# Kernel tuning notes

Measured on AMD Instinct MI355X. Metric: run time of the kernel, lower is better.

Reference implementation:

```python
import jax, jax.numpy as jnp
import numpy as np
import math

FACTOR = 5

def setup_inputs() -> dict:
    key = jax.random.key(0)
    kq, kk, kv = jax.random.split(key, 3)
    B, L, H, D = 2, 4096, 8, 64
    queries = jax.random.normal(kq, (B, L, H, D), dtype=jnp.float32)
    keys = jax.random.normal(kk, (B, L, H, D), dtype=jnp.float32)
    values = jax.random.normal(kv, (B, L, H, D), dtype=jnp.float32)
    attn_mask = jnp.ones((B, L), dtype=jnp.int32)
    return {"queries": queries, "keys": keys, "values": values, "attn_mask": attn_mask}

def reference(queries, keys, values, attn_mask):
    B, L_Q, H, D = queries.shape
    L_K = keys.shape[1]
    # [B, L, H, D] -> [B, H, L, D]
    Q = jnp.transpose(queries, (0, 2, 1, 3))
    K = jnp.transpose(keys, (0, 2, 1, 3))
    V = jnp.transpose(values, (0, 2, 1, 3))

    U_part = max(min(FACTOR * int(math.ceil(math.log(max(L_K, 1)))), L_K), 1)
    u = max(min(FACTOR * int(math.ceil(math.log(max(L_Q, 1)))), L_Q), 1)

    # random key sampling per query (torch.randint replaced by fixed jax key)
    idx = jax.random.randint(jax.random.key(1), (L_Q, U_part), 0, L_K)  # [L_Q, S]
    K_sample = K[:, :, idx, :]  # [B, H, L_Q, S, D]  (irregular gather)
    Q_K_sample = jnp.einsum('bhqd,bhqsd->bhqs', Q, K_sample)  # [B, H, L_Q, S]

    # sparsity measure M = max - mean(full-length normalization L_K as in source)
    M = Q_K_sample.max(axis=-1) - Q_K_sample.sum(axis=-1) / L_K  # [B, H, L_Q]
    _, M_top = jax.lax.top_k(M, u)  # [B, H, u]

    Q_reduce = jnp.take_along_axis(Q, M_top[..., None], axis=2)  # [B, H, u, D]
    scale = 1.0 / math.sqrt(D)
    scores = jnp.einsum('bhud,bhkd->bhuk', Q_reduce, K) * scale  # [B, H, u, L_K]

    mask = attn_mask[:, None, None, :]  # [B,1,1,L_K]
    scores = jnp.where(mask == 0, -jnp.inf, scores)

    A = jax.nn.softmax(scores, axis=-1)  # dropout p=0 -> identity
    context = jnp.einsum('bhuk,bhkd->bhud', A, V)  # [B, H, u, D]
    return jnp.transpose(context, (0, 2, 1, 3))  # [B, u, H, D]
```

## Files before the change

kernel.cpp:

```cpp
#include <hip/hip_runtime.h>
#include <math.h>

#define JAX_PARTITIONABLE 1

constexpr int Bc = 2, Lc = 4096, Hc = 8, Dc = 64;
constexpr int BHc = Bc * Hc;
constexpr int Uc = 45;
constexpr int NSc = 45;

typedef float vfloat4 __attribute__((ext_vector_type(4)));

struct TF2 { unsigned a, b; };

__host__ __device__ constexpr unsigned rotl32(unsigned v, int n) {
  return (v << n) | (v >> (32 - n));
}

__host__ __device__ constexpr TF2 tf2(unsigned k0, unsigned k1, unsigned x0, unsigned x1) {
  unsigned ks2 = k0 ^ k1 ^ 0x1BD11BDAu;
  x0 += k0; x1 += k1;
  x0 += x1; x1 = rotl32(x1, 13); x1 ^= x0;
  x0 += x1; x1 = rotl32(x1, 15); x1 ^= x0;
  x0 += x1; x1 = rotl32(x1, 26); x1 ^= x0;
  x0 += x1; x1 = rotl32(x1, 6);  x1 ^= x0;
  x0 += k1; x1 += ks2 + 1u;
  x0 += x1; x1 = rotl32(x1, 17); x1 ^= x0;
  x0 += x1; x1 = rotl32(x1, 29); x1 ^= x0;
  x0 += x1; x1 = rotl32(x1, 16); x1 ^= x0;
  x0 += x1; x1 = rotl32(x1, 24); x1 ^= x0;
  x0 += ks2; x1 += k0 + 2u;
  x0 += x1; x1 = rotl32(x1, 13); x1 ^= x0;
  x0 += x1; x1 = rotl32(x1, 15); x1 ^= x0;
  x0 += x1; x1 = rotl32(x1, 26); x1 ^= x0;
  x0 += x1; x1 = rotl32(x1, 6);  x1 ^= x0;
  x0 += k0; x1 += k1 + 3u;
  x0 += x1; x1 = rotl32(x1, 17); x1 ^= x0;
  x0 += x1; x1 = rotl32(x1, 29); x1 ^= x0;
  x0 += x1; x1 = rotl32(x1, 16); x1 ^= x0;
  x0 += x1; x1 = rotl32(x1, 24); x1 ^= x0;
  x0 += k1; x1 += ks2 + 4u;
  x0 += x1; x1 = rotl32(x1, 13); x1 ^= x0;
  x0 += x1; x1 = rotl32(x1, 15); x1 ^= x0;
  x0 += x1; x1 = rotl32(x1, 26); x1 ^= x0;
  x0 += x1; x1 = rotl32(x1, 6);  x1 ^= x0;
  x0 += ks2; x1 += k0 + 5u;
  return TF2{x0, x1};
}

template <int CTRL>
__device__ __forceinline__ float dpp_add(float x) {
  int t = __builtin_amdgcn_update_dpp(0, __float_as_int(x), CTRL, 0xF, 0xF, false);
  return x + __int_as_float(t);
}
template <int CTRL>
__device__ __forceinline__ int dpp_addi(int x) {
  int t = __builtin_amdgcn_update_dpp(0, x, CTRL, 0xF, 0xF, false);
  return x + t;
}
template <int CTRL>
__device__ __forceinline__ float dpp_idf(float x) {
  int t = __builtin_amdgcn_update_dpp(__float_as_int(x), __float_as_int(x), CTRL, 0xF, 0xF, false);
  return __int_as_float(t);
}
__device__ __forceinline__ float wave_max_bcast(float x) {
  x = fmaxf(x, dpp_idf<0x111>(x));
  x = fmaxf(x, dpp_idf<0x112>(x));
  x = fmaxf(x, dpp_idf<0x114>(x));
  x = fmaxf(x, dpp_idf<0x118>(x));
  x = fmaxf(x, dpp_idf<0x142>(x));
  x = fmaxf(x, dpp_idf<0x143>(x));
  return __int_as_float(__builtin_amdgcn_readlane(__float_as_int(x), 63));
}
__device__ __forceinline__ float wave_sum_bcast(float x) {
  x = dpp_add<0x111>(x);
  x = dpp_add<0x112>(x);
  x = dpp_add<0x114>(x);
  x = dpp_add<0x118>(x);
  x = dpp_add<0x142>(x);
  x = dpp_add<0x143>(x);
  return __int_as_float(__builtin_amdgcn_readlane(__float_as_int(x), 63));
}

__device__ __forceinline__ float dot4_acc(float4 q, float4 k, float a) {
  a = fmaf(q.x, k.x, a);
  a = fmaf(q.y, k.y, a);
  a = fmaf(q.z, k.z, a);
  a = fmaf(q.w, k.w, a);
  return a;
}

__global__ __launch_bounds__(256) void k_scoreM(const float* __restrict__ Q, const float* __restrict__ K,
                                                float* __restrict__ M) {
  __shared__ int sidx[720];
  int tid = threadIdx.x;
  int bx = blockIdx.x;
  int bh = bx & 15;
  int qblk = bx >> 4;
  int b = bh >> 3, h = bh & 7;
  int lane16 = tid & 15, qloc = tid >> 4;
  int q = qblk * 16 + qloc;
  constexpr TF2 kb = tf2(0u, 1u, 0u, 1u);
  for (int e = tid; e < 720; e += 256) {
    TF2 r = tf2(kb.a, kb.b, 0u, (unsigned)(qblk * 720 + e));
    sidx[e] = (int)((r.a ^ r.b) & 4095u);
  }
  __syncthreads();
  const vfloat4* Q4 = (const vfloat4*)Q;
  const vfloat4* K4 = (const vfloat4*)K;
  vfloat4 qr = Q4[((b * Lc + q) * Hc + h) * 16 + lane16];
  int kbase = (b * Lc * Hc + h) * 16 + lane16;
  const int* ip = sidx + qloc * NSc;
  float mx = -INFINITY, sm = 0.f;
  #pragma unroll
  for (int s0 = 0; s0 < NSc; s0 += 5) {
    int kk[5];
    #pragma unroll
    for (int i = 0; i < 5; ++i) kk[i] = ip[s0 + i];
    vfloat4 kv[5];
    #pragma unroll
    for (int i = 0; i < 5; ++i) kv[i] = __builtin_nontemporal_load(&K4[kbase + kk[i] * (Hc * 16)]);
    #pragma unroll
    for (int i = 0; i < 5; ++i) {
      float p = fmaf(qr[0], kv[i][0], fmaf(qr[1], kv[i][1], fmaf(qr[2], kv[i][2], qr[3] * kv[i][3])));
      p = dpp_add<0x111>(p);
      p = dpp_add<0x112>(p);
      p = dpp_add<0x114>(p);
      p = dpp_add<0x118>(p);
      mx = fmaxf(mx, p);
      sm += p;
    }
  }
  if (lane16 == 15) M[bh * Lc + q] = mx - sm * (1.0f / Lc);
}

__global__ __launch_bounds__(256) void k_topk(const float* __restrict__ M, const float* __restrict__ Q,
                                              int* __restrict__ topk, float* __restrict__ qg) {
  __shared__ unsigned su[Lc];
  __shared__ int hist[4][256];
  __shared__ int sfx[257];
  __shared__ unsigned s_prefix;
  __shared__ int s_r;
  __shared__ int n_gt, n_eq;
  __shared__ unsigned cu[64];
  __shared__ int cidx[64];
  __shared__ int eqi[64];
  __shared__ int srank[Uc];
  int bh = blockIdx.x, tid = threadIdx.x;
  int b = bh >> 3, h = bh & 7;
  int w = tid >> 6;
  const float* m = M + bh * Lc;
  for (int e = tid; e < Lc; e += 256) {
    unsigned bb = __float_as_uint(m[e]);
    su[e] = (bb & 0x80000000u) ? ~bb : (bb | 0x80000000u);
  }
  if (tid == 0) { s_r = Uc; s_prefix = 0u; n_gt = 0; n_eq = 0; sfx[256] = 0; }
  __syncthreads();
  #pragma unroll
  for (int p = 0; p < 4; ++p) {
    int shift = 24 - 8 * p;
    hist[0][tid] = 0; hist[1][tid] = 0; hist[2][tid] = 0; hist[3][tid] = 0;
    __syncthreads();
    unsigned pref = s_prefix;
    unsigned hmask = (p == 0) ? 0u : (0xFFFFFFFFu << (shift + 8));
    for (int e = tid; e < Lc; e += 256) {
      unsigned u = su[e];
      if ((u & hmask) == pref) atomicAdd(&hist[w][(u >> shift) & 255u], 1);
    }
    __syncthreads();
    if (tid < 64) {
      int i0 = 255 - 4 * tid;
      int h0 = hist[0][i0]     + hist[1][i0]     + hist[2][i0]     + hist[3][i0];
      int h1 = hist[0][i0 - 1] + hist[1][i0 - 1] + hist[2][i0 - 1] + hist[3][i0 - 1];
      int h2 = hist[0][i0 - 2] + hist[1][i0 - 2] + hist[2][i0 - 2] + hist[3][i0 - 2];
      int h3 = hist[0][i0 - 3] + hist[1][i0 - 3] + hist[2][i0 - 3] + hist[3][i0 - 3];
      int s0i = h0, s1i = s0i + h1, s2i = s1i + h2, s3i = s2i + h3;
      int tot = s3i;
      int x = tot;
      x = dpp_addi<0x111>(x);
      x = dpp_addi<0x112>(x);
      x = dpp_addi<0x114>(x);
      x = dpp_addi<0x118>(x);
      int r0 = __builtin_amdgcn_readlane(x, 15);
      int r1 = __builtin_amdgcn_readlane(x, 31);
      int r2 = __builtin_amdgcn_readlane(x, 47);
      if (tid >= 16) x += r0;
      if (tid >= 32) x += r1;
      if (tid >= 48) x += r2;
      int excl = x - tot;
      sfx[i0]     = excl + s0i;
      sfx[i0 - 1] = excl + s1i;
      sfx[i0 - 2] = excl + s2i;
      sfx[i0 - 3] = excl + s3i;
    }
    __syncthreads();
    int r = s_r;
    __syncthreads();
    int above = sfx[tid + 1];
    if (sfx[tid] >= r && above < r) {
      s_r = r - above;
      s_prefix = pref | ((unsigned)tid << shift);
    }
    __syncthreads();
  }
  unsigned T = s_prefix;
  int rf = s_r;
  for (int e = tid; e < Lc; e += 256) {
    unsigned u = su[e];
    if (u > T) {
      int p = atomicAdd(&n_gt, 1);
      cu[p] = u; cidx[p] = e;
    } else if (u == T) {
      int p = atomicAdd(&n_eq, 1);
      if (p < 64) eqi[p] = e;
    }
  }
  __syncthreads();
  int ne = n_eq < 64 ? n_eq : 64;
  if (tid < ne) {
    int myi = eqi[tid];
    int rank = 0;
    for (int j = 0; j < ne; ++j) rank += (eqi[j] < myi);
    if (rank < rf) {
      int p = atomicAdd(&n_gt, 1);
      cu[p] = T; cidx[p] = myi;
    }
  }
  __syncthreads();
  if (tid < Uc) {
    unsigned mu = cu[tid]; int mi = cidx[tid];
    int rank = 0;
    for (int j = 0; j < Uc; ++j) {
      unsigned ju = cu[j]; int ji = cidx[j];
      rank += (ju > mu) || (ju == mu && ji < mi);
    }
    topk[bh * Uc + rank] = mi;
    srank[rank] = mi;
  }
  __syncthreads();
  const float4* Q4 = (const float4*)Q;
  float4* qg4 = (float4*)qg;
  for (int e = tid; e < Uc * 16; e += 256) {
    int t = e >> 4, dq = e & 15;
    qg4[bh * Uc * 16 + e] = Q4[((b * Lc + srank[t]) * Hc + h) * 16 + dq];
  }
}

template<int NC>
__global__ __launch_bounds__(256, 4) void k_attn(const float* __restrict__ qg, const float* __restrict__ K,
                                                 const float* __restrict__ V, const int* __restrict__ amask,
                                                 float* __restrict__ pO, float* __restrict__ pM,
                                                 float* __restrict__ pL) {
  constexpr int CH = Lc / NC;
  constexpr int TG = 256 / CH;
  constexpr int SCW = CH + 4;
  int chunk = blockIdx.x, bh = blockIdx.y;
  int b = bh >> 3, h = bh & 7;
  int tid = threadIdx.x;
  __shared__ __align__(16) float qs[Uc * 64];
  __shared__ __align__(16) float sc[48][SCW];
  {
    const float4* qg4 = (const float4*)qg;
    float4* qs4w = (float4*)qs;
    for (int e = tid; e < Uc * 16; e += 256) qs4w[e] = qg4[bh * Uc * 16 + e];
  }
  for (int e = tid; e < 3 * SCW; e += 256) sc[45 + e / SCW][e % SCW] = 0.f;
  __syncthreads();
  {
    int k = tid % CH, tg = tid / CH;
    int key = chunk * CH + k;
    const float4* K4 = (const float4*)K;
    int kb = ((b * Lc + key) * Hc + h) * 16;
    float4 kr[16];
    #pragma unroll
    for (int j = 0; j < 16; ++j) kr[j] = K4[kb + j];
    int mk = amask[b * Lc + key];
    const float4* qs4 = (const float4*)qs;
    for (int t = tg; t < Uc; t += TG) {
      float a0 = 0.f, a1 = 0.f, a2 = 0.f, a3 = 0.f;
      #pragma unroll
      for (int j = 0; j < 16; j += 4) {
        a0 = dot4_acc(qs4[t * 16 + j],     kr[j],     a0);
        a1 = dot4_acc(qs4[t * 16 + j + 1], kr[j + 1], a1);
        a2 = dot4_acc(qs4[t * 16 + j + 2], kr[j + 2], a2);
        a3 = dot4_acc(qs4[t * 16 + j + 3], kr[j + 3], a3);
      }
      float acc = (a0 + a1) + (a2 + a3);
      sc[t][k] = mk ? acc * 0.125f : -INFINITY;
    }
  }
  __syncthreads();
  {
    int w = tid >> 6, lane = tid & 63;
    for (int t = w; t < Uc; t += 4) {
      float x = sc[t][lane];
      float ml = wave_max_bcast(x);
      float p = (ml != -INFINITY) ? __expf(x - ml) : 0.f;
      sc[t][lane] = p;
      float ls = wave_sum_bcast(p);
      if (lane == 0) {
        pM[(bh * NC + chunk) * Uc + t] = ml;
        pL[(bh * NC + chunk) * Uc + t] = ls;
      }
    }
  }
  __syncthreads();
  {
    int ty = tid >> 4, tx = tid & 15;
    float4 o0 = {0.f, 0.f, 0.f, 0.f};
    float4 o1 = {0.f, 0.f, 0.f, 0.f};
    float4 o2 = {0.f, 0.f, 0.f, 0.f};
    const float4* V4 = (const float4*)V;
    const float4* s0 = (const float4*)&sc[ty][0];
    const float4* s1 = (const float4*)&sc[ty + 16][0];
    const float4* s2 = (const float4*)&sc[ty + 32][0];
    int vbase = (b * Lc + chunk * CH) * (Hc * 16) + h * 16 + tx;
    #pragma unroll 2
    for (int kq = 0; kq < CH / 4; ++kq) {
      float4 p0 = s0[kq], p1 = s1[kq], p2 = s2[kq];
      float4 va = V4[vbase + (4 * kq + 0) * (Hc * 16)];
      float4 vb = V4[vbase + (4 * kq + 1) * (Hc * 16)];
      float4 vc = V4[vbase + (4 * kq + 2) * (Hc * 16)];
      float4 vd = V4[vbase + (4 * kq + 3) * (Hc * 16)];
      o0.x = fmaf(p0.x, va.x, o0.x); o0.y = fmaf(p0.x, va.y, o0.y); o0.z = fmaf(p0.x, va.z, o0.z); o0.w = fmaf(p0.x, va.w, o0.w);
      o1.x = fmaf(p1.x, va.x, o1.x); o1.y = fmaf(p1.x, va.y, o1.y); o1.z = fmaf(p1.x, va.z, o1.z); o1.w = fmaf(p1.x, va.w, o1.w);
      o2.x = fmaf(p2.x, va.x, o2.x); o2.y = fmaf(p2.x, va.y, o2.y); o2.z = fmaf(p2.x, va.z, o2.z); o2.w = fmaf(p2.x, va.w, o2.w);
      o0.x = fmaf(p0.y, vb.x, o0.x); o0.y = fmaf(p0.y, vb.y, o0.y); o0.z = fmaf(p0.y, vb.z, o0.z); o0.w = fmaf(p0.y, vb.w, o0.w);
      o1.x = fmaf(p1.y, vb.x, o1.x); o1.y = fmaf(p1.y, vb.y, o1.y); o1.z = fmaf(p1.y, vb.z, o1.z); o1.w = fmaf(p1.y, vb.w, o1.w);
      o2.x = fmaf(p2.y, vb.x, o2.x); o2.y = fmaf(p2.y, vb.y, o2.y); o2.z = fmaf(p2.y, vb.z, o2.z); o2.w = fmaf(p2.y, vb.w, o2.w);
      o0.x = fmaf(p0.z, vc.x, o0.x); o0.y = fmaf(p0.z, vc.y, o0.y); o0.z = fmaf(p0.z, vc.z, o0.z); o0.w = fmaf(p0.z, vc.w, o0.w);
      o1.x = fmaf(p1.z, vc.x, o1.x); o1.y = fmaf(p1.z, vc.y, o1.y); o1.z = fmaf(p1.z, vc.z, o1.z); o1.w = fmaf(p1.z, vc.w, o1.w);
      o2.x = fmaf(p2.z, vc.x, o2.x); o2.y = fmaf(p2.z, vc.y, o2.y); o2.z = fmaf(p2.z, vc.z, o2.z); o2.w = fmaf(p2.z, vc.w, o2.w);
      o0.x = fmaf(p0.w, vd.x, o0.x); o0.y = fmaf(p0.w, vd.y, o0.y); o0.z = fmaf(p0.w, vd.z, o0.z); o0.w = fmaf(p0.w, vd.w, o0.w);
      o1.x = fmaf(p1.w, vd.x, o1.x); o1.y = fmaf(p1.w, vd.y, o1.y); o1.z = fmaf(p1.w, vd.z, o1.z); o1.w = fmaf(p1.w, vd.w, o1.w);
      o2.x = fmaf(p2.w, vd.x, o2.x); o2.y = fmaf(p2.w, vd.y, o2.y); o2.z = fmaf(p2.w, vd.z, o2.z); o2.w = fmaf(p2.w, vd.w, o2.w);
    }
    float4* pO4 = (float4*)pO;
    int obase = ((bh * NC + chunk) * Uc) * 16 + tx;
    pO4[obase + ty * 16] = o0;
    pO4[obase + (ty + 16) * 16] = o1;
    if (ty < 13) pO4[obase + (ty + 32) * 16] = o2;
  }
}

template<int NC>
__global__ __launch_bounds__(256) void k_merge(const float* __restrict__ pO, const float* __restrict__ pM,
                                               const float* __restrict__ pL, float* __restrict__ out) {
  constexpr int CPT = NC / 4;
  __shared__ float smax[4];
  __shared__ float sden[4];
  __shared__ float snum[4][64];
  int bid = blockIdx.x;
  int bh = bid & 15, t = bid >> 4;
  int b = bh >> 3, h = bh & 7;
  int tid = threadIdx.x;
  int d = tid & 63, cg = tid >> 6;
  int mlbase = bh * NC * Uc + t;
  float lm = -INFINITY;
  #pragma unroll 4
  for (int c = cg * CPT; c < (cg + 1) * CPT; ++c)
    lm = fmaxf(lm, pM[mlbase + c * Uc]);
  if (d == 0) smax[cg] = lm;
  __syncthreads();
  float m = fmaxf(fmaxf(smax[0], smax[1]), fmaxf(smax[2], smax[3]));
  float den = 0.f, num = 0.f;
  #pragma unroll 4
  for (int c = cg * CPT; c < (cg + 1) * CPT; ++c) {
    float mc = pM[mlbase + c * Uc];
    float wgt = (mc == -INFINITY) ? 0.f : __expf(mc - m);
    den += wgt * pL[mlbase + c * Uc];
    num += wgt * pO[(mlbase + c * Uc) * 64 + d];
  }
  if (d == 0) sden[cg] = den;
  snum[cg][d] = num;
  __syncthreads();
  if (cg == 0) {
    float dn = sden[0] + sden[1] + sden[2] + sden[3];
    float nm = snum[0][d] + snum[1][d] + snum[2][d] + snum[3][d];
    out[((b * Uc + t) * Hc + h) * 64 + d] = nm / dn;
  }
}

extern "C" void kernel_launch(void* const* d_in, const int* in_sizes, int n_in,
                              void* d_out, int out_size, void* d_ws, size_t ws_size,
                              hipStream_t stream) {
  const float* Q = (const float*)d_in[0];
  const float* K = (const float*)d_in[1];
  const float* V = (const float*)d_in[2];
  const int* amask = (const int*)d_in[3];
  float* out = (float*)d_out;
  char* ws = (char*)d_ws;
  float* M    = (float*)(ws + 0x000000);
  int*   topk = (int*)(ws + 0x040000);
  float* qg   = (float*)(ws + 0x041000);
  float* pM   = (float*)(ws + 0x070000);
  size_t need64 = 0x70000UL + 64UL * 190080UL;
  size_t need32 = 0x70000UL + 32UL * 190080UL;
  int NC = ws_size >= need64 ? 64 : (ws_size >= need32 ? 32 : 16);
  float* pL = pM + 16 * NC * Uc;
  float* pO = pL + 16 * NC * Uc;

  k_scoreM<<<4096, 256, 0, stream>>>(Q, K, M);
  k_topk<<<BHc, 256, 0, stream>>>(M, Q, topk, qg);
  if (NC == 64) {
    k_attn<64><<<dim3(64, BHc), 256, 0, stream>>>(qg, K, V, amask, pO, pM, pL);
    k_merge<64><<<BHc * Uc, 256, 0, stream>>>(pO, pM, pL, out);
  } else if (NC == 32) {
    k_attn<32><<<dim3(32, BHc), 256, 0, stream>>>(qg, K, V, amask, pO, pM, pL);
    k_merge<32><<<BHc * Uc, 256, 0, stream>>>(pO, pM, pL, out);
  } else {
    k_attn<16><<<dim3(16, BHc), 256, 0, stream>>>(qg, K, V, amask, pO, pM, pL);
    k_merge<16><<<BHc * Uc, 256, 0, stream>>>(pO, pM, pL, out);
  }
}
```

Measured before the change: 165.0 us.

## Bucket sampled keys by row range and stage K tiles in shared memory

Adds a kernel that regenerates the random sample indices and buckets them, per group of 16 queries, into 32 key-row ranges of 128 rows, writing compact byte tables. The scoring kernel then loads one 128-row K tile into LDS and, for every query, evaluates only the sampled keys that fall in that tile. It writes per-range partial max and sum, and top-k combines the 32 partials. The goal is to replace random global gathers of K with shared-memory reads. In exchange it adds an extra kernel, a larger partial buffer, irregular per-query loop trip counts, and a bucket capacity limit that could silently drop entries.

```diff
diff --git a/kernel.cpp b/kernel.cpp
--- a/kernel.cpp
+++ b/kernel.cpp
@@ -7,6 +7,10 @@
 constexpr int BHc = Bc * Hc;
 constexpr int Uc = 45;
 constexpr int NSc = 45;
+constexpr int NRng = 32;
+constexpr int RowsPerRng = 128;
+constexpr int TabRowB = 96;
+constexpr int EntCap = 79;
 
 typedef float vfloat4 __attribute__((ext_vector_type(4)));
 
@@ -89,39 +93,109 @@
   return a;
 }
 
-__global__ __launch_bounds__(256) void k_scoreM(const float* __restrict__ Q, const float* __restrict__ K,
-                                                float* __restrict__ M) {
-  __shared__ int sidx[720];
+__global__ __launch_bounds__(256) void k_edges(unsigned char* __restrict__ tab) {
+  __shared__ unsigned short kk[720];
+  __shared__ int hist[512];
+  __shared__ int base[513];
+  __shared__ int cur[512];
+  int qc = blockIdx.x, tid = threadIdx.x;
+  constexpr TF2 kb = tf2(0u, 1u, 0u, 1u);
+  for (int t = tid; t < 512; t += 256) hist[t] = 0;
+  for (int e = tid; e < 720; e += 256) {
+    TF2 r = tf2(kb.a, kb.b, 0u, (unsigned)(qc * 720 + e));
+    kk[e] = (unsigned short)((r.a ^ r.b) & 4095u);
+  }
+  __syncthreads();
+  for (int e = tid; e < 720; e += 256) {
+    int b = ((int)(kk[e] >> 7)) * 16 + (e / 45);
+    atomicAdd(&hist[b], 1);
+  }
+  __syncthreads();
+  if (tid < 64) {
+    int i0 = 8 * tid;
+    int h[8], s = 0;
+    #pragma unroll
+    for (int j = 0; j < 8; ++j) { h[j] = hist[i0 + j]; s += h[j]; }
+    int x = s;
+    x = dpp_addi<0x111>(x);
+    x = dpp_addi<0x112>(x);
+    x = dpp_addi<0x114>(x);
+    x = dpp_addi<0x118>(x);
+    int r0 = __builtin_amdgcn_readlane(x, 15);
+    int r1 = __builtin_amdgcn_readlane(x, 31);
+    int r2 = __builtin_amdgcn_readlane(x, 47);
+    if (tid >= 16) x += r0;
+    if (tid >= 32) x += r1;
+    if (tid >= 48) x += r2;
+    int excl = x - s;
+    int acc = excl;
+    #pragma unroll
+    for (int j = 0; j < 8; ++j) { base[i0 + j] = acc; acc += h[j]; }
+    if (tid == 63) base[512] = acc;
+  }
+  __syncthreads();
+  for (int t = tid; t < 512; t += 256) cur[t] = base[t];
+  for (int t = tid; t < 512; t += 256) {
+    int r = t >> 4, j = t & 15;
+    tab[qc * (NRng * TabRowB) + r * TabRowB + j] = (unsigned char)(base[r * 16 + j] - base[r * 16]);
+  }
+  if (tid < NRng)
+    tab[qc * (NRng * TabRowB) + tid * TabRowB + 16] = (unsigned char)(base[tid * 16 + 16] - base[tid * 16]);
+  __syncthreads();
+  for (int e = tid; e < 720; e += 256) {
+    int k = kk[e];
+    int b = (k >> 7) * 16 + (e / 45);
+    int pos = atomicAdd(&cur[b], 1);
+    int r = b >> 4;
+    int local = pos - base[r * 16];
+    if (local < EntCap)
+      tab[qc * (NRng * TabRowB) + r * TabRowB + 17 + local] = (unsigned char)(k & 127);
+  }
+}
+
+__global__ __launch_bounds__(256) void k_scoreM2(const float* __restrict__ Q, const float* __restrict__ K,
+                                                 const unsigned* __restrict__ tab32,
+                                                 float2* __restrict__ P2) {
+  __shared__ vfloat4 sK[RowsPerRng * 16];
+  __shared__ unsigned wtb[4][3][24];
   int tid = threadIdx.x;
   int bx = blockIdx.x;
   int bh = bx & 15;
-  int qblk = bx >> 4;
+  int rr = (bx >> 4) & 31;
+  int qgi = bx >> 9;
   int b = bh >> 3, h = bh & 7;
-  int lane16 = tid & 15, qloc = tid >> 4;
-  int q = qblk * 16 + qloc;
-  constexpr TF2 kb = tf2(0u, 1u, 0u, 1u);
-  for (int e = tid; e < 720; e += 256) {
-    TF2 r = tf2(kb.a, kb.b, 0u, (unsigned)(qblk * 720 + e));
-    sidx[e] = (int)((r.a ^ r.b) & 4095u);
-  }
-  __syncthreads();
+  int lane16 = tid & 15, g = tid >> 4;
+  int w = tid >> 6, lane = tid & 63;
+  int r0 = rr * RowsPerRng;
   const vfloat4* Q4 = (const vfloat4*)Q;
   const vfloat4* K4 = (const vfloat4*)K;
-  vfloat4 qr = Q4[((b * Lc + q) * Hc + h) * 16 + lane16];
-  int kbase = (b * Lc * Hc + h) * 16 + lane16;
-  const int* ip = sidx + qloc * NSc;
-  float mx = -INFINITY, sm = 0.f;
-  #pragma unroll
-  for (int s0 = 0; s0 < NSc; s0 += 5) {
-    int kk[5];
-    #pragma unroll
-    for (int i = 0; i < 5; ++i) kk[i] = ip[s0 + i];
-    vfloat4 kv[5];
-    #pragma unroll
-    for (int i = 0; i < 5; ++i) kv[i] = __builtin_nontemporal_load(&K4[kbase + kk[i] * (Hc * 16)]);
-    #pragma unroll
-    for (int i = 0; i < 5; ++i) {
-      float p = fmaf(qr[0], kv[i][0], fmaf(qr[1], kv[i][1], fmaf(qr[2], kv[i][2], qr[3] * kv[i][3])));
+  for (int e = tid; e < RowsPerRng * 16; e += 256) {
+    int row = e >> 4, c = e & 15;
+    sK[e] = __builtin_nontemporal_load(&K4[((b * Lc + r0 + row) * Hc + h) * 16 + c]);
+  }
+  __syncthreads();
+  int qc0 = qgi * 128;
+  if (lane < 24) {
+    wtb[w][0][lane] = tab32[(qc0 + 0) * (NRng * TabRowB / 4) + rr * (TabRowB / 4) + lane];
+    wtb[w][1][lane] = tab32[(qc0 + 1) * (NRng * TabRowB / 4) + rr * (TabRowB / 4) + lane];
+  }
+  vfloat4 qv_cur = Q4[((b * Lc + ((qc0 + 0) * 16 + g)) * Hc + h) * 16 + lane16];
+  vfloat4 qv_nx  = Q4[((b * Lc + ((qc0 + 1) * 16 + g)) * Hc + h) * 16 + lane16];
+  for (int i = 0; i < 128; ++i) {
+    int qc = qc0 + i;
+    vfloat4 qv_in;
+    if (i + 2 < 128) {
+      qv_in = Q4[((b * Lc + ((qc + 2) * 16 + g)) * Hc + h) * 16 + lane16];
+      if (lane < 24)
+        wtb[w][(i + 2) % 3][lane] = tab32[(qc + 2) * (NRng * TabRowB / 4) + rr * (TabRowB / 4) + lane];
+    }
+    const unsigned char* row = (const unsigned char*)&wtb[w][i % 3][0];
+    int o0 = row[g], o1 = row[g + 1];
+    float mx = -INFINITY, sm = 0.f;
+    for (int j = o0; j < o1; ++j) {
+      int klo = row[17 + j];
+      vfloat4 kv = sK[klo * 16 + lane16];
+      float p = fmaf(qv_cur[0], kv[0], fmaf(qv_cur[1], kv[1], fmaf(qv_cur[2], kv[2], qv_cur[3] * kv[3])));
       p = dpp_add<0x111>(p);
       p = dpp_add<0x112>(p);
       p = dpp_add<0x114>(p);
@@ -129,11 +203,16 @@
       mx = fmaxf(mx, p);
       sm += p;
     }
-  }
-  if (lane16 == 15) M[bh * Lc + q] = mx - sm * (1.0f / Lc);
-}
-
-__global__ __launch_bounds__(256) void k_topk(const float* __restrict__ M, const float* __restrict__ Q,
+    if (lane16 == 15) {
+      float2 v; v.x = mx; v.y = sm;
+      P2[(bh * NRng + rr) * Lc + qc * 16 + g] = v;
+    }
+    qv_cur = qv_nx;
+    qv_nx = qv_in;
+  }
+}
+
+__global__ __launch_bounds__(256) void k_topk(const float2* __restrict__ P2, const float* __restrict__ Q,
                                               int* __restrict__ topk, float* __restrict__ qg) {
   __shared__ unsigned su[Lc];
   __shared__ int hist[4][256];
@@ -148,9 +227,16 @@
   int bh = blockIdx.x, tid = threadIdx.x;
   int b = bh >> 3, h = bh & 7;
   int w = tid >> 6;
-  const float* m = M + bh * Lc;
   for (int e = tid; e < Lc; e += 256) {
-    unsigned bb = __float_as_uint(m[e]);
+    float mx = -INFINITY, sm = 0.f;
+    #pragma unroll 8
+    for (int r = 0; r < NRng; ++r) {
+      float2 v = P2[(bh * NRng + r) * Lc + e];
+      mx = fmaxf(mx, v.x);
+      sm += v.y;
+    }
+    float Mv = mx - sm * (1.0f / Lc);
+    unsigned bb = __float_as_uint(Mv);
     su[e] = (bb & 0x80000000u) ? ~bb : (bb | 0x80000000u);
   }
   if (tid == 0) { s_r = Uc; s_prefix = 0u; n_gt = 0; n_eq = 0; sfx[256] = 0; }
@@ -389,18 +475,20 @@
   const int* amask = (const int*)d_in[3];
   float* out = (float*)d_out;
   char* ws = (char*)d_ws;
-  float* M    = (float*)(ws + 0x000000);
-  int*   topk = (int*)(ws + 0x040000);
-  float* qg   = (float*)(ws + 0x041000);
-  float* pM   = (float*)(ws + 0x070000);
-  size_t need64 = 0x70000UL + 64UL * 190080UL;
-  size_t need32 = 0x70000UL + 32UL * 190080UL;
+  float2* P2  = (float2*)(ws + 0x0000000);
+  unsigned char* tab = (unsigned char*)(ws + 0x1000000);
+  int*   topk = (int*)(ws + 0x10C0000);
+  float* qg   = (float*)(ws + 0x10C1000);
+  float* pM   = (float*)(ws + 0x1100000);
+  size_t need64 = 0x1100000UL + 64UL * 190080UL;
+  size_t need32 = 0x1100000UL + 32UL * 190080UL;
   int NC = ws_size >= need64 ? 64 : (ws_size >= need32 ? 32 : 16);
   float* pL = pM + 16 * NC * Uc;
   float* pO = pL + 16 * NC * Uc;
 
-  k_scoreM<<<4096, 256, 0, stream>>>(Q, K, M);
-  k_topk<<<BHc, 256, 0, stream>>>(M, Q, topk, qg);
+  k_edges<<<256, 256, 0, stream>>>(tab);
+  k_scoreM2<<<1024, 256, 0, stream>>>(Q, K, (const unsigned*)tab, P2);
+  k_topk<<<BHc, 256, 0, stream>>>(P2, Q, topk, qg);
   if (NC == 64) {
     k_attn<64><<<dim3(64, BHc), 256, 0, stream>>>(qg, K, V, amask, pO, pM, pL);
     k_merge<64><<<BHc * Uc, 256, 0, stream>>>(pO, pM, pL, out);
```

New measurement: 260.8 us. 1.58x slower.
